# Kernel tuning notes

Measured on AMD Instinct MI355X. Metric: run time of the kernel, lower is better.

## Reference

```python
import jax, jax.numpy as jnp
import numpy as np

EMBED_DIM = 1024
NUM_HEADS = 16
HEAD_DIM = EMBED_DIM // NUM_HEADS


def setup_inputs() -> dict:
    key = jax.random.key(0)
    kx, kq, kk, kv, ko = jax.random.split(key, 5)
    B, S = 4, 2048
    std = 1.0 / np.sqrt(EMBED_DIM)
    x = jax.random.normal(kx, (B, S, EMBED_DIM), dtype=jnp.float32)
    # nn.Linear weights stored as [out, in]; applied as x @ W.T
    Wq = jax.random.normal(kq, (EMBED_DIM, EMBED_DIM), dtype=jnp.float32) * std
    Wk = jax.random.normal(kk, (EMBED_DIM, EMBED_DIM), dtype=jnp.float32) * std
    Wv = jax.random.normal(kv, (EMBED_DIM, EMBED_DIM), dtype=jnp.float32) * std
    Wo = jax.random.normal(ko, (EMBED_DIM, EMBED_DIM), dtype=jnp.float32) * std
    return {"x": x, "Wq": Wq, "Wk": Wk, "Wv": Wv, "Wo": Wo}


def reference(x, Wq, Wk, Wv, Wo):
    B, S, E = x.shape
    H, D = NUM_HEADS, HEAD_DIM
    scale = jnp.sqrt(jnp.float32(D))

    def proj(W):
        # x @ W.T -> (B, S, E) -> (B, H, S, D)
        return (x @ W.T).reshape(B, S, H, D).transpose(0, 2, 1, 3)

    q, k, v = proj(Wq), proj(Wk), proj(Wv)
    scores = jnp.einsum("bhsd,bhtd->bhst", q, k) / scale  # (B,H,S,S)
    causal = jnp.tril(jnp.ones((S, S), dtype=bool))
    scores = jnp.where(causal, scores, -jnp.inf)
    attn = jax.nn.softmax(scores, axis=-1)  # dropout in eval mode = identity
    out = jnp.einsum("bhst,bhtd->bhsd", attn, v)  # (B,H,S,D)
    out = out.transpose(0, 2, 1, 3).reshape(B, S, E)
    return out @ Wo.T
```

## Files before the change

### kernel.cpp

```cpp
#include <hip/hip_runtime.h>
#include <stdint.h>

#define NHEADS 16
#define EDIM   1024
#define SEQ    2048
#define BATCH  4

typedef float  floatx4 __attribute__((ext_vector_type(4)));
typedef __bf16 bf16x8  __attribute__((ext_vector_type(8)));
typedef unsigned short u16;

__device__ __forceinline__ u16 f2bf(float f) {
  union { float f; unsigned int u; } v; v.f = f;
  return (u16)((v.u + 0x7fffu + ((v.u >> 16) & 1u)) >> 16);
}

__device__ __forceinline__ unsigned int pkbf(float lo, float hi) {
  union { float f; unsigned int u; } a, c;
  a.f = lo; c.f = hi;
  return __builtin_amdgcn_perm(c.u + 0x8000u, a.u + 0x8000u, 0x07060302u);
}

__device__ __forceinline__ void gl2lds16(const u16* g, u16* l) {
  __builtin_amdgcn_global_load_lds(
      (const __attribute__((address_space(1))) unsigned int*)g,
      (__attribute__((address_space(3))) unsigned int*)l, 16, 0, 0);
}

__global__ void cvt_all(const float* __restrict__ x,  const float* __restrict__ wq,
                        const float* __restrict__ wk, const float* __restrict__ wv,
                        const float* __restrict__ wo, u16* __restrict__ xb,
                        u16* __restrict__ wqkv, u16* __restrict__ wob, float qscale) {
  const float* src; u16* dst; int n4; float sc = 1.f;
  switch (blockIdx.y) {
    case 0: src = x;  dst = xb;             n4 = 2097152; break;
    case 1: src = wq; dst = wqkv;           n4 = 262144; sc = qscale; break;
    case 2: src = wk; dst = wqkv + 1048576; n4 = 262144; break;
    case 3: src = wv; dst = wqkv + 2097152; n4 = 262144; break;
    default: src = wo; dst = wob;           n4 = 262144; break;
  }
  const int stride = gridDim.x * blockDim.x;
  for (int i = blockIdx.x * blockDim.x + threadIdx.x; i < n4; i += stride) {
    float4 f = ((const float4*)src)[i];
    uint2 o;
    o.x = pkbf(f.x * sc, f.y * sc);
    o.y = pkbf(f.z * sc, f.w * sc);
    ((uint2*)dst)[i] = o;
  }
}

template <int MODE>
__global__ __launch_bounds__(256, 3)
void gemm_tn(const u16* __restrict__ A, const u16* __restrict__ B,
             void* __restrict__ Cq, u16* __restrict__ Ck, u16* __restrict__ Cv,
             int Kdim) {
  __shared__ u16 As[128 * 64];
  __shared__ u16 Bs[128 * 64];
  const int tid  = threadIdx.x;
  const int w    = tid >> 6, lane = tid & 63;
  const int quad = lane >> 4, l15 = lane & 15;
  const int sr   = lane >> 3, sc8 = lane & 7;
  const int rowA0 = blockIdx.y * 128, rowB0 = blockIdx.x * 128;
  const int wrow  = (w >> 1) * 64,    wcol  = (w & 1) * 64;

  const floatx4 vzero = {0.f, 0.f, 0.f, 0.f};
  floatx4 acc[4][4];
#pragma unroll
  for (int mi = 0; mi < 4; ++mi)
#pragma unroll
    for (int ni = 0; ni < 4; ++ni) acc[mi][ni] = vzero;

  for (int k0 = 0; k0 < Kdim; k0 += 64) {
    __syncthreads();
#pragma unroll
    for (int i = 0; i < 4; ++i) {
      const int r = w * 32 + i * 8;
      gl2lds16(A + (size_t)(rowA0 + r + sr) * Kdim + k0 + ((sc8 ^ sr) * 8), As + r * 64);
      gl2lds16(B + (size_t)(rowB0 + r + sr) * Kdim + k0 + ((sc8 ^ sr) * 8), Bs + r * 64);
    }
    __syncthreads();
#pragma unroll
    for (int ks = 0; ks < 2; ++ks) {
      bf16x8 af[4], bfr[4];
#pragma unroll
      for (int mi = 0; mi < 4; ++mi)
        af[mi] = *(const bf16x8*)(As + (wrow + mi * 16 + l15) * 64 + (((ks * 4 + quad) ^ (l15 & 7)) * 8));
#pragma unroll
      for (int ni = 0; ni < 4; ++ni)
        bfr[ni] = *(const bf16x8*)(Bs + (wcol + ni * 16 + l15) * 64 + (((ks * 4 + quad) ^ (l15 & 7)) * 8));
#pragma unroll
      for (int mi = 0; mi < 4; ++mi)
#pragma unroll
        for (int ni = 0; ni < 4; ++ni)
          acc[mi][ni] = __builtin_amdgcn_mfma_f32_16x16x32_bf16(af[mi], bfr[ni], acc[mi][ni], 0, 0, 0);
    }
  }

  const int matid = rowA0 >> 10;
#pragma unroll
  for (int mi = 0; mi < 4; ++mi)
#pragma unroll
    for (int ni = 0; ni < 4; ++ni) {
      const int e0 = rowA0 + wrow + mi * 16 + quad * 4;
      const int s  = rowB0 + wcol + ni * 16 + l15;
      if (MODE == 1) {
        *(floatx4*)((float*)Cq + (size_t)s * 1024 + e0) = acc[mi][ni];
      } else {
        const int e_loc = e0 & 1023;
        if (matid < 2) {
          u16* dst = (matid == 0) ? (u16*)Cq : Ck;
          uint2 pk;
          pk.x = pkbf(acc[mi][ni][0], acc[mi][ni][1]);
          pk.y = pkbf(acc[mi][ni][2], acc[mi][ni][3]);
          *(uint2*)(dst + (size_t)s * 1024 + e_loc) = pk;
        } else {
          const int b = s >> 11, s_loc = s & 2047;
#pragma unroll
          for (int r = 0; r < 4; ++r)
            Cv[(size_t)(b * 1024 + e_loc + r) * SEQ + s_loc] = f2bf(acc[mi][ni][r]);
        }
      }
    }
}

__global__ __launch_bounds__(512, 4)
void attn_fwd(const u16* __restrict__ Q, const u16* __restrict__ K,
              const u16* __restrict__ Vt, u16* __restrict__ Ctx) {
  __shared__ u16 Ks[128 * 64];
  __shared__ u16 Vs[64 * 128];
  const int tid  = threadIdx.x;
  const int w    = tid >> 6, lane = tid & 63;
  const int quad = lane >> 4, l15 = lane & 15;
  const int bh = blockIdx.x, b = bh >> 4, h = bh & 15;
  const int p  = blockIdx.y;
  const int qts[2] = {p, 15 - p};

  bf16x8 bq[2][2];
#pragma unroll
  for (int tt = 0; tt < 2; ++tt)
#pragma unroll
    for (int ks = 0; ks < 2; ++ks) {
      const int qs = qts[tt] * 128 + w * 16 + l15;
      bq[tt][ks] = *(const bf16x8*)(Q + (size_t)(b * SEQ + qs) * EDIM + h * 64 + ks * 32 + quad * 8);
    }

  const floatx4 vzero = {0.f, 0.f, 0.f, 0.f};
  floatx4 o_acc[2][4];
  float l_run[2] = {0.f, 0.f};
#pragma unroll
  for (int tt = 0; tt < 2; ++tt)
#pragma unroll
    for (int di = 0; di < 4; ++di) o_acc[tt][di] = vzero;

  const int krow = lane >> 3, kch = lane & 7;
  const int vrow = lane >> 4, vch = lane & 15;

  for (int kt = 0; kt <= qts[1]; ++kt) {
    __syncthreads();
#pragma unroll
    for (int ii = 0; ii < 2; ++ii) {
      const int r0 = w * 16 + ii * 8;
      const int row = r0 + krow;
      gl2lds16(K + (size_t)(b * SEQ + kt * 128 + row) * EDIM + h * 64 + ((kch ^ (row & 7)) * 8),
               Ks + r0 * 64);
      const int d0 = w * 8 + ii * 4;
      const int dd = d0 + vrow;
      gl2lds16(Vt + (size_t)(bh * 64 + dd) * SEQ + kt * 128 + ((vch ^ (dd & 15)) * 8),
               Vs + d0 * 128);
    }
    __syncthreads();

#pragma unroll
    for (int tt = 1; tt >= 0; --tt) {
      if (tt == 0 && kt > qts[0]) continue;

      floatx4 s_acc[8];
#pragma unroll
      for (int mi = 0; mi < 8; ++mi) s_acc[mi] = vzero;
#pragma unroll
      for (int ks = 0; ks < 2; ++ks) {
        bf16x8 ak[8];
#pragma unroll
        for (int mi = 0; mi < 8; ++mi)
          ak[mi] = *(const bf16x8*)(Ks + (mi * 16 + l15) * 64 + (((ks * 4 + quad) ^ (l15 & 7)) * 8));
#pragma unroll
        for (int mi = 0; mi < 8; ++mi)
          s_acc[mi] = __builtin_amdgcn_mfma_f32_16x16x32_bf16(ak[mi], bq[tt][ks], s_acc[mi], 0, 0, 0);
      }

      if (kt == qts[tt]) {
        const int q_loc = w * 16 + l15;
#pragma unroll
        for (int mi = 0; mi < 8; ++mi)
#pragma unroll
          for (int r = 0; r < 4; ++r) {
            const int t_loc = mi * 16 + quad * 4 + r;
            if (t_loc > q_loc) s_acc[mi][r] = -1e30f;
          }
      }

      float ls = 0.f;
      unsigned int pk[4][4];
#pragma unroll
      for (int mi = 0; mi < 8; ++mi) {
        float p0 = __builtin_amdgcn_exp2f(s_acc[mi][0]);
        float p1 = __builtin_amdgcn_exp2f(s_acc[mi][1]);
        float p2 = __builtin_amdgcn_exp2f(s_acc[mi][2]);
        float p3 = __builtin_amdgcn_exp2f(s_acc[mi][3]);
        ls += (p0 + p1) + (p2 + p3);
        pk[mi >> 1][(mi & 1) * 2 + 0] = pkbf(p0, p1);
        pk[mi >> 1][(mi & 1) * 2 + 1] = pkbf(p2, p3);
      }
      ls += __shfl_xor(ls, 16, 64);
      ls += __shfl_xor(ls, 32, 64);
      l_run[tt] += ls;

#pragma unroll
      for (int ks = 0; ks < 4; ++ks) {
        union { unsigned int u[4]; bf16x8 v; } pb;
        pb.u[0] = pk[ks][0]; pb.u[1] = pk[ks][1];
        pb.u[2] = pk[ks][2]; pb.u[3] = pk[ks][3];
        const int cA = ((ks * 4 + (quad >> 1)) ^ l15) * 8 + (quad & 1) * 4;
        const int cB = ((ks * 4 + 2 + (quad >> 1)) ^ l15) * 8 + (quad & 1) * 4;
#pragma unroll
        for (int di = 0; di < 4; ++di) {
          const u16* vrowp = Vs + (di * 16 + l15) * 128;
          union { uint2 u2[2]; bf16x8 v; } va;
          va.u2[0] = *(const uint2*)(vrowp + cA);
          va.u2[1] = *(const uint2*)(vrowp + cB);
          o_acc[tt][di] = __builtin_amdgcn_mfma_f32_16x16x32_bf16(va.v, pb.v, o_acc[tt][di], 0, 0, 0);
        }
      }
    }
  }

#pragma unroll
  for (int tt = 0; tt < 2; ++tt) {
    const float rl = 1.f / l_run[tt];
    const int qs = qts[tt] * 128 + w * 16 + l15;
#pragma unroll
    for (int di = 0; di < 4; ++di) {
      uint2 ov;
      ov.x = pkbf(o_acc[tt][di][0] * rl, o_acc[tt][di][1] * rl);
      ov.y = pkbf(o_acc[tt][di][2] * rl, o_acc[tt][di][3] * rl);
      *(uint2*)(Ctx + (size_t)(b * SEQ + qs) * EDIM + h * 64 + di * 16 + quad * 4) = ov;
    }
  }
}

extern "C" void kernel_launch(void* const* d_in, const int* in_sizes, int n_in,
                              void* d_out, int out_size, void* d_ws, size_t ws_size,
                              hipStream_t stream) {
  const float* x  = (const float*)d_in[0];
  const float* Wq = (const float*)d_in[1];
  const float* Wk = (const float*)d_in[2];
  const float* Wv = (const float*)d_in[3];
  const float* Wo = (const float*)d_in[4];
  float* out = (float*)d_out;
  u16* ws = (u16*)d_ws;

  const size_t ME = (size_t)BATCH * SEQ * EDIM;
  u16* Xb   = ws;
  u16* Wqkv = Xb + ME;
  u16* Wob  = Wqkv + 3u * 1024 * 1024;
  u16* Qb   = Wob + 1024u * 1024;
  u16* Kb   = Qb + ME;
  u16* Vtr  = Kb + ME;
  u16* Ctx  = Vtr + ME;

  const float qscale = 0.125f * 1.44269504f;

  cvt_all<<<dim3(512, 5), 256, 0, stream>>>(x, Wq, Wk, Wv, Wo, Xb, Wqkv, Wob, qscale);
  gemm_tn<0><<<dim3(64, 24), 256, 0, stream>>>(Wqkv, Xb, (void*)Qb, Kb, Vtr, EDIM);
  attn_fwd<<<dim3(64, 8), 512, 0, stream>>>(Qb, Kb, Vtr, Ctx);
  gemm_tn<1><<<dim3(64, 8), 256, 0, stream>>>(Wob, Ctx, (void*)out, nullptr, nullptr, EDIM);
}
```

Baseline: 255.6 us.

## Double-buffer K/V tiles in attention and vectorize transposed V projection stores

The attention kernel now keeps two LDS buffers for K and V. The next tile's global-to-LDS copy is issued right after the barrier, so it overlaps with the current tile's MFMA work, and one barrier per iteration is removed. The QKV GEMM swaps MFMA operands for the V slice so each lane holds four consecutive sequence positions, which replaces the 2-byte scattered transposed stores with packed 8-byte stores. The GEMM launch-bounds occupancy hint also drops from 3 to 2. Doubling attention LDS to 64KB per block reduces how many blocks fit per CU, so there is less latency hiding from occupancy in exchange for the explicit prefetch.

```diff
diff --git a/kernel.cpp b/kernel.cpp
--- a/kernel.cpp
+++ b/kernel.cpp
@@ -50,7 +50,7 @@
 }
 
 template <int MODE>
-__global__ __launch_bounds__(256, 3)
+__global__ __launch_bounds__(256, 2)
 void gemm_tn(const u16* __restrict__ A, const u16* __restrict__ B,
              void* __restrict__ Cq, u16* __restrict__ Ck, u16* __restrict__ Cv,
              int Kdim) {
@@ -62,6 +62,7 @@
   const int sr   = lane >> 3, sc8 = lane & 7;
   const int rowA0 = blockIdx.y * 128, rowB0 = blockIdx.x * 128;
   const int wrow  = (w >> 1) * 64,    wcol  = (w & 1) * 64;
+  const int matid = (MODE == 0) ? (rowA0 >> 10) : 1;
 
   const floatx4 vzero = {0.f, 0.f, 0.f, 0.f};
   floatx4 acc[4][4];
@@ -88,37 +89,47 @@
 #pragma unroll
       for (int ni = 0; ni < 4; ++ni)
         bfr[ni] = *(const bf16x8*)(Bs + (wcol + ni * 16 + l15) * 64 + (((ks * 4 + quad) ^ (l15 & 7)) * 8));
-#pragma unroll
-      for (int mi = 0; mi < 4; ++mi)
-#pragma unroll
-        for (int ni = 0; ni < 4; ++ni)
-          acc[mi][ni] = __builtin_amdgcn_mfma_f32_16x16x32_bf16(af[mi], bfr[ni], acc[mi][ni], 0, 0, 0);
-    }
-  }
-
-  const int matid = rowA0 >> 10;
+      if (MODE == 0 && matid == 2) {
+#pragma unroll
+        for (int mi = 0; mi < 4; ++mi)
+#pragma unroll
+          for (int ni = 0; ni < 4; ++ni)
+            acc[mi][ni] = __builtin_amdgcn_mfma_f32_16x16x32_bf16(bfr[ni], af[mi], acc[mi][ni], 0, 0, 0);
+      } else {
+#pragma unroll
+        for (int mi = 0; mi < 4; ++mi)
+#pragma unroll
+          for (int ni = 0; ni < 4; ++ni)
+            acc[mi][ni] = __builtin_amdgcn_mfma_f32_16x16x32_bf16(af[mi], bfr[ni], acc[mi][ni], 0, 0, 0);
+      }
+    }
+  }
+
 #pragma unroll
   for (int mi = 0; mi < 4; ++mi)
 #pragma unroll
     for (int ni = 0; ni < 4; ++ni) {
-      const int e0 = rowA0 + wrow + mi * 16 + quad * 4;
-      const int s  = rowB0 + wcol + ni * 16 + l15;
       if (MODE == 1) {
+        const int e0 = rowA0 + wrow + mi * 16 + quad * 4;
+        const int s  = rowB0 + wcol + ni * 16 + l15;
         *(floatx4*)((float*)Cq + (size_t)s * 1024 + e0) = acc[mi][ni];
+      } else if (matid < 2) {
+        const int e0 = rowA0 + wrow + mi * 16 + quad * 4;
+        const int s  = rowB0 + wcol + ni * 16 + l15;
+        const int e_loc = e0 & 1023;
+        u16* dst = (matid == 0) ? (u16*)Cq : Ck;
+        uint2 pk;
+        pk.x = pkbf(acc[mi][ni][0], acc[mi][ni][1]);
+        pk.y = pkbf(acc[mi][ni][2], acc[mi][ni][3]);
+        *(uint2*)(dst + (size_t)s * 1024 + e_loc) = pk;
       } else {
-        const int e_loc = e0 & 1023;
-        if (matid < 2) {
-          u16* dst = (matid == 0) ? (u16*)Cq : Ck;
-          uint2 pk;
-          pk.x = pkbf(acc[mi][ni][0], acc[mi][ni][1]);
-          pk.y = pkbf(acc[mi][ni][2], acc[mi][ni][3]);
-          *(uint2*)(dst + (size_t)s * 1024 + e_loc) = pk;
-        } else {
-          const int b = s >> 11, s_loc = s & 2047;
-#pragma unroll
-          for (int r = 0; r < 4; ++r)
-            Cv[(size_t)(b * 1024 + e_loc + r) * SEQ + s_loc] = f2bf(acc[mi][ni][r]);
-        }
+        const int e_loc = (rowA0 + wrow + mi * 16 + l15) & 1023;
+        const int s_full = rowB0 + wcol + ni * 16 + quad * 4;
+        const int bb = s_full >> 11, s_loc = s_full & 2047;
+        uint2 pk;
+        pk.x = pkbf(acc[mi][ni][0], acc[mi][ni][1]);
+        pk.y = pkbf(acc[mi][ni][2], acc[mi][ni][3]);
+        *(uint2*)(Cv + (size_t)(bb * 1024 + e_loc) * SEQ + s_loc) = pk;
       }
     }
 }
@@ -126,14 +137,15 @@
 __global__ __launch_bounds__(512, 4)
 void attn_fwd(const u16* __restrict__ Q, const u16* __restrict__ K,
               const u16* __restrict__ Vt, u16* __restrict__ Ctx) {
-  __shared__ u16 Ks[128 * 64];
-  __shared__ u16 Vs[64 * 128];
+  __shared__ u16 Ks[2][128 * 64];
+  __shared__ u16 Vs[2][64 * 128];
   const int tid  = threadIdx.x;
   const int w    = tid >> 6, lane = tid & 63;
   const int quad = lane >> 4, l15 = lane & 15;
   const int bh = blockIdx.x, b = bh >> 4, h = bh & 15;
   const int p  = blockIdx.y;
   const int qts[2] = {p, 15 - p};
+  const int kmax = qts[1];
 
   bf16x8 bq[2][2];
 #pragma unroll
@@ -155,20 +167,31 @@
   const int krow = lane >> 3, kch = lane & 7;
   const int vrow = lane >> 4, vch = lane & 15;
 
-  for (int kt = 0; kt <= qts[1]; ++kt) {
+#define STAGE_KV(buf, ktn)                                                          \
+  {                                                                                 \
+    _Pragma("unroll")                                                               \
+    for (int ii = 0; ii < 2; ++ii) {                                                \
+      const int r0 = w * 16 + ii * 8;                                               \
+      const int row = r0 + krow;                                                    \
+      gl2lds16(K + (size_t)(b * SEQ + (ktn) * 128 + row) * EDIM + h * 64 +          \
+                   ((kch ^ (row & 7)) * 8),                                         \
+               &Ks[buf][r0 * 64]);                                                  \
+      const int d0 = w * 8 + ii * 4;                                                \
+      const int dd = d0 + vrow;                                                     \
+      gl2lds16(Vt + (size_t)(bh * 64 + dd) * SEQ + (ktn) * 128 +                    \
+                   ((vch ^ (dd & 15)) * 8),                                         \
+               &Vs[buf][d0 * 128]);                                                 \
+    }                                                                               \
+  }
+
+  STAGE_KV(0, 0);
+
+  for (int kt = 0; kt <= kmax; ++kt) {
+    const int cur = kt & 1;
     __syncthreads();
-#pragma unroll
-    for (int ii = 0; ii < 2; ++ii) {
-      const int r0 = w * 16 + ii * 8;
-      const int row = r0 + krow;
-      gl2lds16(K + (size_t)(b * SEQ + kt * 128 + row) * EDIM + h * 64 + ((kch ^ (row & 7)) * 8),
-               Ks + r0 * 64);
-      const int d0 = w * 8 + ii * 4;
-      const int dd = d0 + vrow;
-      gl2lds16(Vt + (size_t)(bh * 64 + dd) * SEQ + kt * 128 + ((vch ^ (dd & 15)) * 8),
-               Vs + d0 * 128);
-    }
-    __syncthreads();
+    if (kt < kmax) STAGE_KV(cur ^ 1, kt + 1);
+    const u16* Ksc = &Ks[cur][0];
+    const u16* Vsc = &Vs[cur][0];
 
 #pragma unroll
     for (int tt = 1; tt >= 0; --tt) {
@@ -182,7 +205,7 @@
         bf16x8 ak[8];
 #pragma unroll
         for (int mi = 0; mi < 8; ++mi)
-          ak[mi] = *(const bf16x8*)(Ks + (mi * 16 + l15) * 64 + (((ks * 4 + quad) ^ (l15 & 7)) * 8));
+          ak[mi] = *(const bf16x8*)(Ksc + (mi * 16 + l15) * 64 + (((ks * 4 + quad) ^ (l15 & 7)) * 8));
 #pragma unroll
         for (int mi = 0; mi < 8; ++mi)
           s_acc[mi] = __builtin_amdgcn_mfma_f32_16x16x32_bf16(ak[mi], bq[tt][ks], s_acc[mi], 0, 0, 0);
@@ -224,7 +247,7 @@
         const int cB = ((ks * 4 + 2 + (quad >> 1)) ^ l15) * 8 + (quad & 1) * 4;
 #pragma unroll
         for (int di = 0; di < 4; ++di) {
-          const u16* vrowp = Vs + (di * 16 + l15) * 128;
+          const u16* vrowp = Vsc + (di * 16 + l15) * 128;
           union { uint2 u2[2]; bf16x8 v; } va;
           va.u2[0] = *(const uint2*)(vrowp + cA);
           va.u2[1] = *(const uint2*)(vrowp + cB);
@@ -246,6 +269,7 @@
       *(uint2*)(Ctx + (size_t)(b * SEQ + qs) * EDIM + h * 64 + di * 16 + quad * 4) = ov;
     }
   }
+#undef STAGE_KV
 }
 
 extern "C" void kernel_launch(void* const* d_in, const int* in_sizes, int n_in,
```

New measurement: 254.0 us. No clear change (-0.6%).
